# Optimization experiments

Measured on AMD Instinct MI355X. Metric: run time of the kernel, lower is better.

## Reference

```python
import jax, jax.numpy as jnp
import numpy as np

EPS = 1e-07
B, N, L, K = 256, 512, 4, 1

def setup_inputs() -> dict:
    key = jax.random.key(0)
    k1, k2, k3, k4 = jax.random.split(key, 4)
    x = jax.random.randint(k1, (B, N), 0, L)
    W = jax.random.normal(k2, (N, N), dtype=jnp.float32)
    V_compress = jax.random.normal(k3, (N, L), dtype=jnp.float32)
    E_compress = jax.random.normal(k4, (K, N, N, L, L), dtype=jnp.float32)
    return {"x": x, "W": W, "V_compress": V_compress, "E_compress": E_compress}

def reference(x, W, V_compress, E_compress):
    n = W.shape[0]
    # V: per-variable marginals via softmax over classes
    V = jax.nn.softmax(V_compress, axis=1)                      # (n, l)
    # E: pairwise joints for mixture 0, normalized over (l, l)
    E = jnp.exp(E_compress[0])                                   # (n, n, l, l)
    E = E / E.sum(axis=(-2, -1), keepdims=True)
    A_b = V[:, None, :, None]                                    # row target marginals
    B_b = V[None, :, None, :]                                    # col target marginals
    # IPFP: 2 iterations of row/col marginal rescaling
    for _ in range(2):
        E = E * (A_b / E.sum(axis=3, keepdims=True))
        E = E * (B_b / E.sum(axis=2, keepdims=True))
        E = E / E.sum(axis=(-2, -1), keepdims=True)
    # zero the diagonal blocks and clamp
    E_mask = (1.0 - jnp.eye(n, dtype=E.dtype))[:, :, None, None]
    E = jnp.clip(E * E_mask, 0.0, 1.0)
    # symmetric edge-weight matrix from W
    Ws = jax.nn.sigmoid(W)
    Ws = jnp.tril(Ws, -1)
    Ws = Ws.T + Ws
    L_0 = -Ws + jnp.diag(Ws.sum(axis=1))                         # (n, n)
    # gather per-sample marginals and pairwise joints
    idx = jnp.arange(n)
    Pr = V[idx[None, :], x]                                      # (B, n): Pr[b,i] = V[i, x[b,i]]
    P = E[idx[:, None], idx[None, :], x[:, :, None], x[:, None, :]]  # (B, n, n)
    P = P / (Pr[:, :, None] * Pr[:, None, :])
    WP = Ws[None, :, :] * P                                      # (B, n, n)
    Lap = -WP + jnp.eye(n, dtype=WP.dtype)[None] * WP.sum(axis=2)[:, :, None]
    # matrix-tree: logdet of the (n-1)x(n-1) minor
    _, ld = jnp.linalg.slogdet(Lap[:, 1:, 1:] + EPS)
    _, ld0 = jnp.linalg.slogdet(L_0[1:, 1:] + EPS)
    y = jnp.log(Pr + EPS).sum(axis=1) + ld - ld0                 # (B,)
    return y
```

## Files before the change

### kernel.cpp

```cpp
#include <hip/hip_runtime.h>

#define NN 512
#define NR 511
#define NB 64
#define BATCH 256
#define NMAT 257
#define EPSF 1e-7f
#define NN2 ((size_t)NN * NN)

__device__ __forceinline__ float block_reduce_sum_512(float v, float* red) {
#pragma unroll
  for (int off = 32; off > 0; off >>= 1) v += __shfl_down(v, off, 64);
  int tid = threadIdx.x;
  if ((tid & 63) == 0) red[tid >> 6] = v;
  __syncthreads();
  float s = 0.f;
#pragma unroll
  for (int w = 0; w < 8; ++w) s += red[w];
  return s;
}

__global__ void k_softmaxV(const float* __restrict__ Vc, float* __restrict__ V) {
  int i = threadIdx.x;
  float v0 = Vc[i * 4 + 0], v1 = Vc[i * 4 + 1], v2 = Vc[i * 4 + 2], v3 = Vc[i * 4 + 3];
  float mx = fmaxf(fmaxf(v0, v1), fmaxf(v2, v3));
  float e0 = expf(v0 - mx), e1 = expf(v1 - mx), e2 = expf(v2 - mx), e3 = expf(v3 - mx);
  float s = e0 + e1 + e2 + e3;
  V[i * 4 + 0] = e0 / s; V[i * 4 + 1] = e1 / s; V[i * 4 + 2] = e2 / s; V[i * 4 + 3] = e3 / s;
}

__global__ void k_Ws(const float* __restrict__ W, float* __restrict__ Ws) {
  int i = blockIdx.x, j = threadIdx.x;
  float v = 0.f;
  if (i != j) {
    int hi = i > j ? i : j, lo = i > j ? j : i;
    float wv = W[hi * NN + lo];
    v = 1.f / (1.f + expf(-wv));
  }
  Ws[i * NN + j] = v;
}

__global__ void k_E(const float* __restrict__ Ec, const float* __restrict__ V,
                    float* __restrict__ E) {
  int idx = blockIdx.x * blockDim.x + threadIdx.x;
  if (idx >= NN * NN) return;
  int i = idx >> 9, j = idx & 511;
  float e[16];
  const float* src = Ec + (size_t)idx * 16;
#pragma unroll
  for (int t = 0; t < 16; ++t) e[t] = expf(src[t]);
  float tot = 0.f;
#pragma unroll
  for (int t = 0; t < 16; ++t) tot += e[t];
  float rt = 1.f / tot;
#pragma unroll
  for (int t = 0; t < 16; ++t) e[t] *= rt;
  float Vi[4], Vj[4];
#pragma unroll
  for (int a = 0; a < 4; ++a) { Vi[a] = V[i * 4 + a]; Vj[a] = V[j * 4 + a]; }
#pragma unroll
  for (int it = 0; it < 2; ++it) {
#pragma unroll
    for (int a = 0; a < 4; ++a) {
      float rs = e[a * 4 + 0] + e[a * 4 + 1] + e[a * 4 + 2] + e[a * 4 + 3];
      float sc = Vi[a] / rs;
#pragma unroll
      for (int b = 0; b < 4; ++b) e[a * 4 + b] *= sc;
    }
#pragma unroll
    for (int b = 0; b < 4; ++b) {
      float cs = e[0 + b] + e[4 + b] + e[8 + b] + e[12 + b];
      float sc = Vj[b] / cs;
#pragma unroll
      for (int a = 0; a < 4; ++a) e[a * 4 + b] *= sc;
    }
    float t2 = 0.f;
#pragma unroll
    for (int t = 0; t < 16; ++t) t2 += e[t];
    float rt2 = 1.f / t2;
#pragma unroll
    for (int t = 0; t < 16; ++t) e[t] *= rt2;
  }
  bool diag = (i == j);
#pragma unroll
  for (int t = 0; t < 16; ++t) {
    float v = diag ? 0.f : e[t];
    E[(size_t)t * NN2 + idx] = fminf(fmaxf(v, 0.f), 1.f);
  }
}

__global__ __launch_bounds__(512)
void k_Pr(const int* __restrict__ x, const float* __restrict__ V,
          float* __restrict__ rPr, float* __restrict__ logPr) {
  __shared__ float red[8];
  int b = blockIdx.x, i = threadIdx.x;
  int xi = x[b * NN + i];
  float pr = V[i * 4 + xi];
  rPr[b * NN + i] = 1.f / pr;
  float s = block_reduce_sum_512(logf(pr + EPSF), red);
  if (i == 0) logPr[b] = s;
}

__global__ __launch_bounds__(512)
void k_build(const int* __restrict__ x, const float* __restrict__ Ws,
             const float* __restrict__ E, const float* __restrict__ rPr,
             float* __restrict__ mats, int m0) {
  int slot = blockIdx.y;
  int m = m0 + slot;
  float* A = mats + (size_t)slot * NN2;
  int wv = threadIdx.x >> 6, lane = threadIdx.x & 63;
  int r = blockIdx.x * 8 + wv;
  float* dst = A + (size_t)r * NN + lane * 8;
  if (r == NR) {
    float4 z0 = {0.f, 0.f, 0.f, 0.f};
    float4 z1 = {0.f, 0.f, 0.f, 0.f};
    if (lane == 63) z1.w = 1.f;
    *(float4*)dst = z0;
    *(float4*)(dst + 4) = z1;
    return;
  }
  int i = r + 1;
  int j0 = lane * 8;
  float4 wsa = *(const float4*)&Ws[i * NN + j0];
  float4 wsb = *(const float4*)&Ws[i * NN + j0 + 4];
  float wp[8];
  if (m < BATCH) {
    const int* xm = x + (size_t)m * NN;
    int xi = xm[i];
    int4 xa = *(const int4*)&xm[j0];
    int4 xb = *(const int4*)&xm[j0 + 4];
    const float* rp = rPr + (size_t)m * NN;
    float rpi = rp[i];
    float4 ra = *(const float4*)&rp[j0];
    float4 rb = *(const float4*)&rp[j0 + 4];
    const float* Eb = E + (size_t)(xi * 4) * NN2 + (size_t)i * NN + j0;
    wp[0] = wsa.x * Eb[(size_t)xa.x * NN2 + 0] * (rpi * ra.x);
    wp[1] = wsa.y * Eb[(size_t)xa.y * NN2 + 1] * (rpi * ra.y);
    wp[2] = wsa.z * Eb[(size_t)xa.z * NN2 + 2] * (rpi * ra.z);
    wp[3] = wsa.w * Eb[(size_t)xa.w * NN2 + 3] * (rpi * ra.w);
    wp[4] = wsb.x * Eb[(size_t)xb.x * NN2 + 4] * (rpi * rb.x);
    wp[5] = wsb.y * Eb[(size_t)xb.y * NN2 + 5] * (rpi * rb.y);
    wp[6] = wsb.z * Eb[(size_t)xb.z * NN2 + 6] * (rpi * rb.z);
    wp[7] = wsb.w * Eb[(size_t)xb.w * NN2 + 7] * (rpi * rb.w);
  } else {
    wp[0] = wsa.x; wp[1] = wsa.y; wp[2] = wsa.z; wp[3] = wsa.w;
    wp[4] = wsb.x; wp[5] = wsb.y; wp[6] = wsb.z; wp[7] = wsb.w;
  }
  float rs = ((wp[0] + wp[1]) + (wp[2] + wp[3])) + ((wp[4] + wp[5]) + (wp[6] + wp[7]));
#pragma unroll
  for (int o = 32; o > 0; o >>= 1) rs += __shfl_xor(rs, o, 64);
  float nxt = __shfl_down(wp[0], 1, 64);
  float sh[8] = {wp[1], wp[2], wp[3], wp[4], wp[5], wp[6], wp[7], nxt};
  float out[8];
#pragma unroll
  for (int t = 0; t < 8; ++t) {
    int c = j0 + t;
    float v = -sh[t] + EPSF;
    if (c == r) v += rs;
    if (c == NR) v = 0.f;
    out[t] = v;
  }
  float4 o0 = {out[0], out[1], out[2], out[3]};
  float4 o1 = {out[4], out[5], out[6], out[7]};
  *(float4*)dst = o0;
  *(float4*)(dst + 4) = o1;
}

template <int S>
struct PStepF {
  static __device__ __forceinline__ void run(float (&rr)[64], float (*Prow)[64],
                                             bool own, int tid, float& lgsum) {
    float rinv = 1.f / Prow[S & 1][S];
    if (own && tid > S) {
      float l = rr[S] * rinv;
      rr[S] = l;
      constexpr int C0 = S + 1;
      constexpr int A4 = (C0 + 3) & ~3;
#pragma unroll
      for (int c = C0; c < (A4 < 64 ? A4 : 64); ++c)
        rr[c] = fmaf(-l, Prow[S & 1][c], rr[c]);
#pragma unroll
      for (int g = A4 / 4; g < 16; ++g) {
        float4 u = *(const float4*)&Prow[S & 1][g * 4];
        rr[g * 4 + 0] = fmaf(-l, u.x, rr[g * 4 + 0]);
        rr[g * 4 + 1] = fmaf(-l, u.y, rr[g * 4 + 1]);
        rr[g * 4 + 2] = fmaf(-l, u.z, rr[g * 4 + 2]);
        rr[g * 4 + 3] = fmaf(-l, u.w, rr[g * 4 + 3]);
      }
    }
    if (S + 1 < 64) {
      if (tid == S + 1) {
        lgsum += logf(rr[S + 1]);
#pragma unroll
        for (int c4 = (S + 1) >> 2; c4 < 16; ++c4) {
          float4 v = {rr[c4 * 4 + 0], rr[c4 * 4 + 1], rr[c4 * 4 + 2], rr[c4 * 4 + 3]};
          *(float4*)&Prow[(S + 1) & 1][c4 * 4] = v;
        }
      }
    }
    __syncthreads();
    PStepF<S + 1>::run(rr, Prow, own, tid, lgsum);
  }
};
template <>
struct PStepF<64> {
  static __device__ __forceinline__ void run(float (&)[64], float (*)[64],
                                             bool, int, float&) {}
};

template <int Q>
struct UStep {
  static __device__ __forceinline__ void run(float (&a)[64], const float* L) {
    constexpr int j0 = Q * 4;
    a[j0 + 1] = fmaf(-L[(j0 + 1) * 68 + j0], a[j0], a[j0 + 1]);
    a[j0 + 2] = fmaf(-L[(j0 + 2) * 68 + j0], a[j0], a[j0 + 2]);
    a[j0 + 2] = fmaf(-L[(j0 + 2) * 68 + j0 + 1], a[j0 + 1], a[j0 + 2]);
    a[j0 + 3] = fmaf(-L[(j0 + 3) * 68 + j0], a[j0], a[j0 + 3]);
    a[j0 + 3] = fmaf(-L[(j0 + 3) * 68 + j0 + 1], a[j0 + 1], a[j0 + 3]);
    a[j0 + 3] = fmaf(-L[(j0 + 3) * 68 + j0 + 2], a[j0 + 2], a[j0 + 3]);
#pragma unroll
    for (int t = j0 + 4; t < 64; ++t) {
      float4 Lv = *(const float4*)&L[t * 68 + j0];
      float v = a[t];
      v = fmaf(-Lv.x, a[j0 + 0], v);
      v = fmaf(-Lv.y, a[j0 + 1], v);
      v = fmaf(-Lv.z, a[j0 + 2], v);
      v = fmaf(-Lv.w, a[j0 + 3], v);
      a[t] = v;
    }
    UStep<Q + 1>::run(a, L);
  }
};
template <>
struct UStep<16> {
  static __device__ __forceinline__ void run(float (&)[64], const float*) {}
};

__global__ __launch_bounds__(512)
void k_pu(float* __restrict__ mats, float* __restrict__ ld, int m0, int p) {
  __shared__ __align__(16) float L11[64 * 68];
  __shared__ __align__(16) float Prow[2][64];
  __shared__ float red[8];
  int slot = blockIdx.x;
  float* A = mats + (size_t)slot * NN2;
  int tid = threadIdx.x;
  int k0 = p * NB;
  int m = NN - k0;
  int w = m - NB;
  bool own = tid < m;
  float* myrow = A + (size_t)(k0 + tid) * NN + k0;
  float lgsum = 0.f;
  float rr[64];

  if (own) {
#pragma unroll
    for (int c4 = 0; c4 < 16; ++c4) {
      float4 v = *(const float4*)(myrow + c4 * 4);
      rr[c4 * 4 + 0] = v.x; rr[c4 * 4 + 1] = v.y;
      rr[c4 * 4 + 2] = v.z; rr[c4 * 4 + 3] = v.w;
    }
  } else {
#pragma unroll
    for (int c = 0; c < 64; ++c) rr[c] = 0.f;
  }
  if (tid == 0) {
    lgsum += logf(rr[0]);
#pragma unroll
    for (int c4 = 0; c4 < 16; ++c4) {
      float4 v = {rr[c4 * 4 + 0], rr[c4 * 4 + 1], rr[c4 * 4 + 2], rr[c4 * 4 + 3]};
      *(float4*)&Prow[0][c4 * 4] = v;
    }
  }
  __syncthreads();
  PStepF<0>::run(rr, Prow, own, tid, lgsum);
  if (own) {
#pragma unroll
    for (int c4 = 0; c4 < 16; ++c4) {
      float4 v = {rr[c4 * 4 + 0], rr[c4 * 4 + 1], rr[c4 * 4 + 2], rr[c4 * 4 + 3]};
      *(float4*)(myrow + c4 * 4) = v;
    }
  }
  if (tid < 64) {
#pragma unroll
    for (int c4 = 0; c4 < 16; ++c4) {
      float4 v = {rr[c4 * 4 + 0], rr[c4 * 4 + 1], rr[c4 * 4 + 2], rr[c4 * 4 + 3]};
      *(float4*)&L11[tid * 68 + c4 * 4] = v;
    }
  }
  __syncthreads();

  if (w > 0 && tid < w) {
    int col = k0 + NB + tid;
#pragma unroll
    for (int t = 0; t < 64; ++t) rr[t] = A[(size_t)(k0 + t) * NN + col];
    UStep<0>::run(rr, L11);
#pragma unroll
    for (int t = 0; t < 64; ++t) A[(size_t)(k0 + t) * NN + col] = rr[t];
  }

  float s = block_reduce_sum_512(lgsum, red);
  if (tid == 0) {
    int gi = m0 + slot;
    if (p == 0) ld[gi] = s;
    else        ld[gi] += s;
  }
}

__global__ __launch_bounds__(256)
void k_gemm(float* __restrict__ mats, int p) {
  __shared__ __align__(16) float At[64 * 132];
  int k0 = p * NB;
  int w = NN - k0 - NB;
  float* A = mats + (size_t)blockIdx.z * NN2;
  int rb = blockIdx.x * 128, cb = blockIdx.y * 128;
  int tid = threadIdx.x;
#pragma unroll
  for (int it = 0; it < 32; ++it) {
    int idx = tid + it * 256;
    int r = idx >> 6, kk = idx & 63;
    int gr = rb + r;
    float v = 0.f;
    if (gr < w) v = A[(size_t)(k0 + NB + gr) * NN + k0 + kk];
    At[kk * 132 + r] = v;
  }
  __syncthreads();
  int ty = tid >> 4, tx = tid & 15;
  int r0 = ty * 8, c0 = tx * 8;
  int gc0 = k0 + NB + cb + c0;
  bool cok = (cb + c0) < w;
  float acc[8][8];
#pragma unroll
  for (int q = 0; q < 8; ++q)
#pragma unroll
    for (int u = 0; u < 8; ++u) acc[q][u] = 0.f;
  float4 bc0 = {0.f, 0.f, 0.f, 0.f}, bc1 = {0.f, 0.f, 0.f, 0.f};
  float4 bn0 = {0.f, 0.f, 0.f, 0.f}, bn1 = {0.f, 0.f, 0.f, 0.f};
  if (cok) {
    const float* Br = &A[(size_t)k0 * NN + gc0];
    bc0 = *(const float4*)Br;
    bc1 = *(const float4*)(Br + 4);
    const float* Br1 = &A[(size_t)(k0 + 1) * NN + gc0];
    bn0 = *(const float4*)Br1;
    bn1 = *(const float4*)(Br1 + 4);
  }
#pragma unroll 2
  for (int kk = 0; kk < 64; ++kk) {
    float4 bf0 = {0.f, 0.f, 0.f, 0.f}, bf1 = {0.f, 0.f, 0.f, 0.f};
    if (cok && kk < 62) {
      const float* Br = &A[(size_t)(k0 + kk + 2) * NN + gc0];
      bf0 = *(const float4*)Br;
      bf1 = *(const float4*)(Br + 4);
    }
    float4 a0 = *(const float4*)&At[kk * 132 + r0];
    float4 a1 = *(const float4*)&At[kk * 132 + r0 + 4];
    float la[8] = {a0.x, a0.y, a0.z, a0.w, a1.x, a1.y, a1.z, a1.w};
    float lb[8] = {bc0.x, bc0.y, bc0.z, bc0.w, bc1.x, bc1.y, bc1.z, bc1.w};
#pragma unroll
    for (int q = 0; q < 8; ++q)
#pragma unroll
      for (int u = 0; u < 8; ++u) acc[q][u] = fmaf(la[q], lb[u], acc[q][u]);
    bc0 = bn0; bc1 = bn1;
    bn0 = bf0; bn1 = bf1;
  }
  if (!cok) return;
#pragma unroll
  for (int q = 0; q < 8; ++q) {
    int gr = rb + r0 + q;
    if (gr < w) {
      float* dst = &A[(size_t)(k0 + NB + gr) * NN + gc0];
      float4 v0 = *(const float4*)dst;
      float4 v1 = *(const float4*)(dst + 4);
      v0.x -= acc[q][0]; v0.y -= acc[q][1]; v0.z -= acc[q][2]; v0.w -= acc[q][3];
      v1.x -= acc[q][4]; v1.y -= acc[q][5]; v1.z -= acc[q][6]; v1.w -= acc[q][7];
      *(float4*)dst = v0;
      *(float4*)(dst + 4) = v1;
    }
  }
}

__global__ void k_y(const float* __restrict__ logPr, const float* __restrict__ ld,
                    float* __restrict__ y) {
  int b = threadIdx.x;
  if (b < BATCH) y[b] = logPr[b] + ld[b] - ld[BATCH];
}

extern "C" void kernel_launch(void* const* d_in, const int* in_sizes, int n_in,
                              void* d_out, int out_size, void* d_ws, size_t ws_size,
                              hipStream_t stream) {
  const int* x = (const int*)d_in[0];
  const float* W = (const float*)d_in[1];
  const float* Vc = (const float*)d_in[2];
  const float* Ec = (const float*)d_in[3];
  float* out = (float*)d_out;

  char* ws = (char*)d_ws;
  size_t off = 0;
  auto alloc = [&](size_t bytes) -> void* {
    void* pp = ws + off;
    off = (off + bytes + 255) & ~(size_t)255;
    return pp;
  };
  float* V     = (float*)alloc((size_t)NN * 4 * 4);
  float* Wsbuf = (float*)alloc(NN2 * 4);
  float* rPr   = (float*)alloc((size_t)BATCH * NN * 4);
  float* logPr = (float*)alloc((size_t)BATCH * 4);
  float* ld    = (float*)alloc((size_t)NMAT * 4);
  float* E     = (float*)alloc(NN2 * 16 * 4);
  size_t per_mat = NN2 * 4;
  size_t remain = ws_size > off ? ws_size - off : 0;
  int cap = (int)(remain / per_mat);
  if (cap > NMAT) cap = NMAT;
  if (cap > 129) cap = 129;
  if (cap < 1) cap = 1;
  float* mats = (float*)(ws + off);

  k_softmaxV<<<1, 512, 0, stream>>>(Vc, V);
  k_Ws<<<NN, NN, 0, stream>>>(W, Wsbuf);
  k_E<<<(NN * NN) / 256, 256, 0, stream>>>(Ec, V, E);
  k_Pr<<<BATCH, NN, 0, stream>>>(x, V, rPr, logPr);

  for (int m0 = 0; m0 < NMAT; m0 += cap) {
    int cnt = NMAT - m0 < cap ? NMAT - m0 : cap;
    dim3 gb(64, cnt);
    k_build<<<gb, 512, 0, stream>>>(x, Wsbuf, E, rPr, mats, m0);
    for (int p = 0; p < 8; ++p) {
      k_pu<<<cnt, 512, 0, stream>>>(mats, ld, m0, p);
      int w = NN - p * NB - NB;
      if (w > 0) {
        int nt = (w + 127) / 128;
        dim3 gg(nt, nt, cnt);
        k_gemm<<<gg, 256, 0, stream>>>(mats, p);
      }
    }
  }
  k_y<<<1, 256, 0, stream>>>(logPr, ld, out);
}
```

Before: 1.642 ms.

## Block panel LU factorization into groups of four rows with wave-level sync

Restructures the 64-column panel factorization in k_pu so pivot rows are published four at a time. Inside each group of four, the owning lanes of the first wave factor the rows in sequence using only wave barriers. The other threads then apply all four updates after a single block barrier, so the number of __syncthreads per panel drops from 64 to 16. The cost is a serial critical path within wave 0 and the reliance on wave-barrier ordering for correctness. The 1/pivot value is now computed once and stored in shared memory.

```diff
diff --git a/kernel.cpp b/kernel.cpp
--- a/kernel.cpp
+++ b/kernel.cpp
@@ -7,6 +7,8 @@
 #define NMAT 257
 #define EPSF 1e-7f
 #define NN2 ((size_t)NN * NN)
+
+#define WSYNC() do { __builtin_amdgcn_wave_barrier(); asm volatile("" ::: "memory"); } while (0)
 
 __device__ __forceinline__ float block_reduce_sum_512(float v, float* red) {
 #pragma unroll
@@ -166,46 +168,85 @@
   *(float4*)(dst + 4) = o1;
 }
 
-template <int S>
-struct PStepF {
-  static __device__ __forceinline__ void run(float (&rr)[64], float (*Prow)[64],
+template <int R>
+__device__ __forceinline__ void apply_row(float (&rr)[64], const float* Prow,
+                                          float rinv) {
+  float l = rr[R] * rinv;
+  rr[R] = l;
+  constexpr int C0 = R + 1;
+  constexpr int A4 = (C0 + 3) & ~3;
+#pragma unroll
+  for (int c = C0; c < (A4 < 64 ? A4 : 64); ++c)
+    rr[c] = fmaf(-l, Prow[c], rr[c]);
+#pragma unroll
+  for (int g = A4 / 4; g < 16; ++g) {
+    float4 u = *(const float4*)&Prow[g * 4];
+    rr[g * 4 + 0] = fmaf(-l, u.x, rr[g * 4 + 0]);
+    rr[g * 4 + 1] = fmaf(-l, u.y, rr[g * 4 + 1]);
+    rr[g * 4 + 2] = fmaf(-l, u.z, rr[g * 4 + 2]);
+    rr[g * 4 + 3] = fmaf(-l, u.w, rr[g * 4 + 3]);
+  }
+}
+
+template <int R>
+__device__ __forceinline__ void publish_row(const float (&rr)[64], float* prow,
+                                            float* pinv, float& lgsum) {
+  lgsum += logf(rr[R]);
+  *pinv = 1.f / rr[R];
+#pragma unroll
+  for (int g = R / 4; g < 16; ++g) {
+    float4 v = {rr[g * 4 + 0], rr[g * 4 + 1], rr[g * 4 + 2], rr[g * 4 + 3]};
+    *(float4*)&prow[g * 4] = v;
+  }
+}
+
+template <int Q>
+struct PStep4 {
+  static __device__ __forceinline__ void run(float (&rr)[64],
+                                             float (*P4)[4][64], float (*Pi)[4],
                                              bool own, int tid, float& lgsum) {
-    float rinv = 1.f / Prow[S & 1][S];
-    if (own && tid > S) {
-      float l = rr[S] * rinv;
-      rr[S] = l;
-      constexpr int C0 = S + 1;
-      constexpr int A4 = (C0 + 3) & ~3;
-#pragma unroll
-      for (int c = C0; c < (A4 < 64 ? A4 : 64); ++c)
-        rr[c] = fmaf(-l, Prow[S & 1][c], rr[c]);
-#pragma unroll
-      for (int g = A4 / 4; g < 16; ++g) {
-        float4 u = *(const float4*)&Prow[S & 1][g * 4];
-        rr[g * 4 + 0] = fmaf(-l, u.x, rr[g * 4 + 0]);
-        rr[g * 4 + 1] = fmaf(-l, u.y, rr[g * 4 + 1]);
-        rr[g * 4 + 2] = fmaf(-l, u.z, rr[g * 4 + 2]);
-        rr[g * 4 + 3] = fmaf(-l, u.w, rr[g * 4 + 3]);
-      }
-    }
-    if (S + 1 < 64) {
-      if (tid == S + 1) {
-        lgsum += logf(rr[S + 1]);
-#pragma unroll
-        for (int c4 = (S + 1) >> 2; c4 < 16; ++c4) {
-          float4 v = {rr[c4 * 4 + 0], rr[c4 * 4 + 1], rr[c4 * 4 + 2], rr[c4 * 4 + 3]};
-          *(float4*)&Prow[(S + 1) & 1][c4 * 4] = v;
-        }
+    if (Q >= 1) {
+      constexpr int G = Q - 1;
+      constexpr int pp = G & 1;
+      if (own && tid > 4 * G + 3) {
+        apply_row<4 * G + 0>(rr, P4[pp][0], Pi[pp][0]);
+        apply_row<4 * G + 1>(rr, P4[pp][1], Pi[pp][1]);
+        apply_row<4 * G + 2>(rr, P4[pp][2], Pi[pp][2]);
+        apply_row<4 * G + 3>(rr, P4[pp][3], Pi[pp][3]);
+      }
+    }
+    {
+      constexpr int par = Q & 1;
+      if (tid == 4 * Q + 0) {
+        publish_row<4 * Q + 0>(rr, P4[par][0], &Pi[par][0], lgsum);
+      }
+      WSYNC();
+      if (tid == 4 * Q + 1) {
+        apply_row<4 * Q + 0>(rr, P4[par][0], Pi[par][0]);
+        publish_row<4 * Q + 1>(rr, P4[par][1], &Pi[par][1], lgsum);
+      }
+      WSYNC();
+      if (tid == 4 * Q + 2) {
+        apply_row<4 * Q + 0>(rr, P4[par][0], Pi[par][0]);
+        apply_row<4 * Q + 1>(rr, P4[par][1], Pi[par][1]);
+        publish_row<4 * Q + 2>(rr, P4[par][2], &Pi[par][2], lgsum);
+      }
+      WSYNC();
+      if (tid == 4 * Q + 3) {
+        apply_row<4 * Q + 0>(rr, P4[par][0], Pi[par][0]);
+        apply_row<4 * Q + 1>(rr, P4[par][1], Pi[par][1]);
+        apply_row<4 * Q + 2>(rr, P4[par][2], Pi[par][2]);
+        publish_row<4 * Q + 3>(rr, P4[par][3], &Pi[par][3], lgsum);
       }
     }
     __syncthreads();
-    PStepF<S + 1>::run(rr, Prow, own, tid, lgsum);
+    PStep4<Q + 1>::run(rr, P4, Pi, own, tid, lgsum);
   }
 };
 template <>
-struct PStepF<64> {
-  static __device__ __forceinline__ void run(float (&)[64], float (*)[64],
-                                             bool, int, float&) {}
+struct PStep4<16> {
+  static __device__ __forceinline__ void run(float (&)[64], float (*)[4][64],
+                                             float (*)[4], bool, int, float&) {}
 };
 
 template <int Q>
@@ -239,7 +280,8 @@
 __global__ __launch_bounds__(512)
 void k_pu(float* __restrict__ mats, float* __restrict__ ld, int m0, int p) {
   __shared__ __align__(16) float L11[64 * 68];
-  __shared__ __align__(16) float Prow[2][64];
+  __shared__ __align__(16) float P4[2][4][64];
+  __shared__ float Pi[2][4];
   __shared__ float red[8];
   int slot = blockIdx.x;
   float* A = mats + (size_t)slot * NN2;
@@ -263,17 +305,14 @@
 #pragma unroll
     for (int c = 0; c < 64; ++c) rr[c] = 0.f;
   }
-  if (tid == 0) {
-    lgsum += logf(rr[0]);
-#pragma unroll
-    for (int c4 = 0; c4 < 16; ++c4) {
-      float4 v = {rr[c4 * 4 + 0], rr[c4 * 4 + 1], rr[c4 * 4 + 2], rr[c4 * 4 + 3]};
-      *(float4*)&Prow[0][c4 * 4] = v;
-    }
-  }
-  __syncthreads();
-  PStepF<0>::run(rr, Prow, own, tid, lgsum);
-  if (own) {
+  PStep4<0>::run(rr, P4, Pi, own, tid, lgsum);
+  if (own && tid > 63) {
+    apply_row<60>(rr, P4[1][0], Pi[1][0]);
+    apply_row<61>(rr, P4[1][1], Pi[1][1]);
+    apply_row<62>(rr, P4[1][2], Pi[1][2]);
+    apply_row<63>(rr, P4[1][3], Pi[1][3]);
+  }
+  if (own && tid >= 64) {
 #pragma unroll
     for (int c4 = 0; c4 < 16; ++c4) {
       float4 v = {rr[c4 * 4 + 0], rr[c4 * 4 + 1], rr[c4 * 4 + 2], rr[c4 * 4 + 3]};
```

After: 1.752 ms. +6.7%, slower.
